# Optimization experiments

Hardware: AMD Instinct MI355X
Metric: run time of the kernel (lower is better)

## Reference

```python
import jax, jax.numpy as jnp
import numpy as np

EPS = 1e-05
KERNEL_SIZE = 9
KERNEL_VOL = float(KERNEL_SIZE ** 3)

_DN = ("NDHWC", "DHWIO", "NDHWC")


def _box_sum(x, k=KERNEL_SIZE):
    """Sliding-window sum over a k^3 box with SAME zero padding.

    The TF module uses a dense all-ones (k,k,k) conv3d; an all-ones kernel is
    separable, so three 1D passes compute the identical result with O(k) work.
    x: (B, D1, D2, D3, 1) float.
    """
    for kshape in ((k, 1, 1), (1, k, 1), (1, 1, k)):
        w = jnp.ones(kshape + (1, 1), dtype=x.dtype)
        x = jax.lax.conv_general_dilated(
            x, w, window_strides=(1, 1, 1), padding="SAME",
            dimension_numbers=_DN)
    return x


def setup_inputs() -> dict:
    key = jax.random.key(0)
    k1, k2 = jax.random.split(key)
    shape = (2, 192, 192, 192)
    y_true = jax.random.uniform(k1, shape, dtype=jnp.float32)
    y_pred = jax.random.uniform(k2, shape, dtype=jnp.float32)
    return {"y_true": y_true, "y_pred": y_pred}


def reference(y_true, y_pred):
    # Expand (B, D1, D2, D3) -> (B, D1, D2, D3, 1) as in the TF call().
    if y_true.ndim == 4:
        y_true = y_true[..., None]
        y_pred = y_pred[..., None]

    t_sum = _box_sum(y_true)
    p_sum = _box_sum(y_pred)
    tp_sum = _box_sum(y_true * y_pred)

    t_avg = t_sum / KERNEL_VOL
    p_avg = p_sum / KERNEL_VOL

    cross = tp_sum - p_avg * t_sum
    num = cross * cross + EPS  # the DEBUG1 variant returns `num` directly
    return num
```

## Files before the change

### kernel.cpp

```cpp
#include <hip/hip_runtime.h>


#define N 192
#define TILE 32
#define ZCHUNK 32
#define NT 6
#define NZC 6

__global__ __launch_bounds__(1024, 4)
void lncc_kernel(const float* __restrict__ t_in,
                 const float* __restrict__ p_in,
                 float* __restrict__ out)
{
    __shared__ __align__(16) float rowT[3 * 32 * 44];
    __shared__ float pcol[3 * 32 * 32];

    const int bid = blockIdx.x;
    const int b   = bid / (NT * NT * NZC);
    int rem       = bid % (NT * NT * NZC);
    const int zc  = rem / (NT * NT);
    rem           = rem % (NT * NT);
    const int ty  = rem / NT;
    const int tx  = rem % NT;

    const int x0 = tx * TILE, y0 = ty * TILE, z0 = zc * ZCHUNK;
    const int tid = threadIdx.x;

    const int  lf   = tid / 320;
    const int  ls   = tid - lf * 320;
    const int  lry  = ls >> 3;
    const int  lxq  = ls & 7;
    const int  lgy  = y0 - 4 + lry;
    const int  lgx0 = x0 - 4 + 4 * lxq;
    const bool lactive = (tid < 960);
    const bool lyok = ((unsigned)lgy < (unsigned)N);

    const int  cf = tid >> 8;
    const int  cyq = (tid >> 5) & 7;
    const int  cx  = tid & 31;
    const bool cactive = (tid < 768);

    const int gx = tid & 31;
    const int gy = tid >> 5;

    const size_t plane = (size_t)N * N;
    const float* tb = t_in + (size_t)b * N * plane;
    const float* pb = p_in + (size_t)b * N * plane;
    float*       ob = out  + (size_t)b * N * plane;

    float ring_t[9], ring_p[9], ring_tp[9];
    float sum_t = 0.f, sum_p = 0.f, sum_tp = 0.f;
    #pragma unroll
    for (int i = 0; i < 9; ++i) { ring_t[i] = 0.f; ring_p[i] = 0.f; ring_tp[i] = 0.f; }

    #pragma unroll 1
    for (int k = 0; k < 5; ++k) {
      #pragma unroll
      for (int r = 0; r < 9; ++r) {
        const int zi = k * 9 + r;
        const int zp = z0 - 4 + zi;
        const bool pvalid = (zi < ZCHUNK + 8) && ((unsigned)zp < (unsigned)N);
        float Pt = 0.f, Pp = 0.f, Ptp = 0.f;
        if (pvalid) {
          if (lactive) {
            const float* rt = tb + (size_t)zp * plane + (size_t)lgy * N;
            const float* rp = pb + (size_t)zp * plane + (size_t)lgy * N;
            float v[12];
            #pragma unroll
            for (int q = 0; q < 3; ++q) {
              const int gxq = lgx0 + 4 * q;
              const bool ok = lyok && ((unsigned)gxq < (unsigned)N);
              float4 a = make_float4(0.f, 0.f, 0.f, 0.f);
              float4 c = make_float4(0.f, 0.f, 0.f, 0.f);
              if (ok) {
                if (lf != 1) a = *(const float4*)(rt + gxq);
                if (lf != 0) c = *(const float4*)(rp + gxq);
              }
              if (lf == 1) a = c;
              if (lf == 2) { a.x *= c.x; a.y *= c.y; a.z *= c.z; a.w *= c.w; }
              v[4*q+0] = a.x; v[4*q+1] = a.y; v[4*q+2] = a.z; v[4*q+3] = a.w;
            }
            float s0 = ((v[0]+v[1]) + (v[2]+v[3])) + ((v[4]+v[5]) + (v[6]+v[7])) + v[8];
            float s1 = s0 - v[0] + v[9];
            float s2 = s1 - v[1] + v[10];
            float s3 = s2 - v[2] + v[11];
            const int wb = (lf * 32 + 4 * lxq) * 44 + lry;
            rowT[wb      ] = s0;
            rowT[wb +  44] = s1;
            rowT[wb +  88] = s2;
            rowT[wb + 132] = s3;
          }
          __syncthreads();
          if (cactive) {
            const float4* rq = (const float4*)&rowT[(cf * 32 + cx) * 44 + 4 * cyq];
            const float4 A = rq[0], B4 = rq[1], C4 = rq[2];
            const float w0=A.x,  w1=A.y,  w2=A.z,  w3=A.w;
            const float w4=B4.x, w5=B4.y, w6=B4.z, w7=B4.w;
            const float w8=C4.x, w9=C4.y, w10=C4.z, w11=C4.w;
            float c0 = ((w0+w1)+(w2+w3)) + ((w4+w5)+(w6+w7)) + w8;
            float c1 = c0 - w0 + w9;
            float c2 = c1 - w1 + w10;
            float c3 = c2 - w2 + w11;
            const int pbase = cf * 1024 + (4 * cyq) * 32 + cx;
            pcol[pbase     ] = c0;
            pcol[pbase + 32] = c1;
            pcol[pbase + 64] = c2;
            pcol[pbase + 96] = c3;
          }
          __syncthreads();
          Pt  = pcol[       gy * 32 + gx];
          Pp  = pcol[1024 + gy * 32 + gx];
          Ptp = pcol[2048 + gy * 32 + gx];
        }
        sum_t  += Pt  - ring_t[r];  ring_t[r]  = Pt;
        sum_p  += Pp  - ring_p[r];  ring_p[r]  = Pp;
        sum_tp += Ptp - ring_tp[r]; ring_tp[r] = Ptp;
        if (zi >= 8 && zi < ZCHUNK + 8) {
          const int zout = zp - 4;
          const float cross = sum_tp - (sum_p * (1.0f / 729.0f)) * sum_t;
          ob[(size_t)zout * plane + (size_t)(y0 + gy) * N + (x0 + gx)]
              = cross * cross + 1e-5f;
        }
      }
    }
}

extern "C" void kernel_launch(void* const* d_in, const int* in_sizes, int n_in,
                              void* d_out, int out_size, void* d_ws, size_t ws_size,
                              hipStream_t stream) {
    const float* y_true = (const float*)d_in[0];
    const float* y_pred = (const float*)d_in[1];
    float* out = (float*)d_out;
    dim3 grid(2 * NT * NT * NZC);
    dim3 block(1024);
    hipLaunchKernelGGL(lncc_kernel, grid, block, 0, stream, y_true, y_pred, out);
}
```

Baseline: 240.6 us.

## Prefetch next z-plane into registers and rebalance z-chunks across a 512-block grid

Loads for plane z+1 are now issued into registers before the shared-memory row/column passes of plane z, so global-load latency overlaps the LDS work and barriers. The grid changes from 432 blocks to 512 blocks with uneven z-chunk sizes (24, 28 or 27 planes), chosen so the block count matches a multiple of the CU count and no wave is left partly idle. The row-transposed LDS stride goes from 44 to 46, with float2 reads, to change the bank-conflict pattern. In exchange it uses more registers for the prefetch buffers and adds more halo recomputation per output plane because the chunks are smaller.

```diff
diff --git a/kernel.cpp b/kernel.cpp
--- a/kernel.cpp
+++ b/kernel.cpp
@@ -2,28 +2,32 @@
 
 
 #define N 192
-#define TILE 32
-#define ZCHUNK 32
-#define NT 6
-#define NZC 6
+#define RSTRIDE 46
 
 __global__ __launch_bounds__(1024, 4)
 void lncc_kernel(const float* __restrict__ t_in,
                  const float* __restrict__ p_in,
                  float* __restrict__ out)
 {
-    __shared__ __align__(16) float rowT[3 * 32 * 44];
+    __shared__ __align__(16) float rowT[3 * 32 * RSTRIDE];
     __shared__ float pcol[3 * 32 * 32];
 
     const int bid = blockIdx.x;
-    const int b   = bid / (NT * NT * NZC);
-    int rem       = bid % (NT * NT * NZC);
-    const int zc  = rem / (NT * NT);
-    rem           = rem % (NT * NT);
-    const int ty  = rem / NT;
-    const int tx  = rem % NT;
-
-    const int x0 = tx * TILE, y0 = ty * TILE, z0 = zc * ZCHUNK;
+    int xy, Z, z0;
+    if (bid < 64) {
+        xy = bid >> 3;
+        Z  = 24;
+        z0 = (bid & 7) * 24;
+    } else {
+        const int q  = bid - 64;
+        xy = 8 + q / 7;
+        const int zi = q % 7;
+        if (zi < 3) { Z = 28; z0 = zi * 28; }
+        else        { Z = 27; z0 = 84 + (zi - 3) * 27; }
+    }
+    const int b  = xy / 36;
+    const int t6 = xy % 36;
+    const int y0 = (t6 / 6) * 32, x0 = (t6 % 6) * 32;
     const int tid = threadIdx.x;
 
     const int  lf   = tid / 320;
@@ -35,7 +39,7 @@
     const bool lactive = (tid < 960);
     const bool lyok = ((unsigned)lgy < (unsigned)N);
 
-    const int  cf = tid >> 8;
+    const int  cf  = tid >> 8;
     const int  cyq = (tid >> 5) & 7;
     const int  cx  = tid & 31;
     const bool cactive = (tid < 768);
@@ -46,80 +50,134 @@
     const size_t plane = (size_t)N * N;
     const float* tb = t_in + (size_t)b * N * plane;
     const float* pb = p_in + (size_t)b * N * plane;
-    float*       ob = out  + (size_t)b * N * plane;
+    float*       ob = out  + (size_t)b * N * plane
+                           + (size_t)(y0 + gy) * N + (x0 + gx);
 
     float ring_t[9], ring_p[9], ring_tp[9];
     float sum_t = 0.f, sum_p = 0.f, sum_tp = 0.f;
     #pragma unroll
     for (int i = 0; i < 9; ++i) { ring_t[i] = 0.f; ring_p[i] = 0.f; ring_tp[i] = 0.f; }
 
+    const float4 z4 = make_float4(0.f, 0.f, 0.f, 0.f);
+    float4 cur0 = z4, cur1 = z4, cur2 = z4;
+
+    {
+        const int zp0 = z0 - 4;
+        if (((unsigned)zp0 < (unsigned)N) && lactive && lyok) {
+            const float* rt = tb + (size_t)zp0 * plane + (size_t)lgy * N;
+            const float* rp = pb + (size_t)zp0 * plane + (size_t)lgy * N;
+            float4 a[3], c[3];
+            #pragma unroll
+            for (int q = 0; q < 3; ++q) {
+                a[q] = z4; c[q] = z4;
+                const int gxq = lgx0 + 4 * q;
+                if ((unsigned)gxq < (unsigned)N) {
+                    a[q] = (lf == 1) ? *(const float4*)(rp + gxq)
+                                     : *(const float4*)(rt + gxq);
+                    if (lf == 2) c[q] = *(const float4*)(rp + gxq);
+                }
+            }
+            if (lf == 2) {
+                #pragma unroll
+                for (int q = 0; q < 3; ++q) {
+                    a[q].x *= c[q].x; a[q].y *= c[q].y;
+                    a[q].z *= c[q].z; a[q].w *= c[q].w;
+                }
+            }
+            cur0 = a[0]; cur1 = a[1]; cur2 = a[2];
+        }
+    }
+
     #pragma unroll 1
-    for (int k = 0; k < 5; ++k) {
+    for (int k = 0; k < 4; ++k) {
       #pragma unroll
       for (int r = 0; r < 9; ++r) {
-        const int zi = k * 9 + r;
-        const int zp = z0 - 4 + zi;
-        const bool pvalid = (zi < ZCHUNK + 8) && ((unsigned)zp < (unsigned)N);
-        float Pt = 0.f, Pp = 0.f, Ptp = 0.f;
-        if (pvalid) {
-          if (lactive) {
-            const float* rt = tb + (size_t)zp * plane + (size_t)lgy * N;
-            const float* rp = pb + (size_t)zp * plane + (size_t)lgy * N;
-            float v[12];
-            #pragma unroll
-            for (int q = 0; q < 3; ++q) {
-              const int gxq = lgx0 + 4 * q;
-              const bool ok = lyok && ((unsigned)gxq < (unsigned)N);
-              float4 a = make_float4(0.f, 0.f, 0.f, 0.f);
-              float4 c = make_float4(0.f, 0.f, 0.f, 0.f);
-              if (ok) {
-                if (lf != 1) a = *(const float4*)(rt + gxq);
-                if (lf != 0) c = *(const float4*)(rp + gxq);
-              }
-              if (lf == 1) a = c;
-              if (lf == 2) { a.x *= c.x; a.y *= c.y; a.z *= c.z; a.w *= c.w; }
-              v[4*q+0] = a.x; v[4*q+1] = a.y; v[4*q+2] = a.z; v[4*q+3] = a.w;
+        const int i  = k * 9 + r;
+        const int zp = z0 - 4 + i;
+        const int zn = zp + 1;
+        const bool vi = (i < Z + 8)     && ((unsigned)zp < (unsigned)N);
+        const bool vn = (i + 1 < Z + 8) && ((unsigned)zn < (unsigned)N);
+
+        float4 fa0 = z4, fa1 = z4, fa2 = z4, fc0 = z4, fc1 = z4, fc2 = z4;
+        if (vn && lactive && lyok) {
+            const float* rt = tb + (size_t)zn * plane + (size_t)lgy * N;
+            const float* rp = pb + (size_t)zn * plane + (size_t)lgy * N;
+            const int g0 = lgx0, g1 = lgx0 + 4, g2 = lgx0 + 8;
+            if ((unsigned)g0 < (unsigned)N) {
+                fa0 = (lf == 1) ? *(const float4*)(rp + g0) : *(const float4*)(rt + g0);
+                if (lf == 2) fc0 = *(const float4*)(rp + g0);
             }
-            float s0 = ((v[0]+v[1]) + (v[2]+v[3])) + ((v[4]+v[5]) + (v[6]+v[7])) + v[8];
-            float s1 = s0 - v[0] + v[9];
-            float s2 = s1 - v[1] + v[10];
-            float s3 = s2 - v[2] + v[11];
-            const int wb = (lf * 32 + 4 * lxq) * 44 + lry;
-            rowT[wb      ] = s0;
-            rowT[wb +  44] = s1;
-            rowT[wb +  88] = s2;
-            rowT[wb + 132] = s3;
-          }
-          __syncthreads();
-          if (cactive) {
-            const float4* rq = (const float4*)&rowT[(cf * 32 + cx) * 44 + 4 * cyq];
-            const float4 A = rq[0], B4 = rq[1], C4 = rq[2];
-            const float w0=A.x,  w1=A.y,  w2=A.z,  w3=A.w;
-            const float w4=B4.x, w5=B4.y, w6=B4.z, w7=B4.w;
-            const float w8=C4.x, w9=C4.y, w10=C4.z, w11=C4.w;
+            if ((unsigned)g1 < (unsigned)N) {
+                fa1 = (lf == 1) ? *(const float4*)(rp + g1) : *(const float4*)(rt + g1);
+                if (lf == 2) fc1 = *(const float4*)(rp + g1);
+            }
+            if ((unsigned)g2 < (unsigned)N) {
+                fa2 = (lf == 1) ? *(const float4*)(rp + g2) : *(const float4*)(rt + g2);
+                if (lf == 2) fc2 = *(const float4*)(rp + g2);
+            }
+        }
+
+        if (vi && lactive) {
+            const float v0 = cur0.x, v1 = cur0.y, v2  = cur0.z, v3  = cur0.w;
+            const float v4 = cur1.x, v5 = cur1.y, v6  = cur1.z, v7  = cur1.w;
+            const float v8 = cur2.x, v9 = cur2.y, v10 = cur2.z, v11 = cur2.w;
+            float s0 = ((v0+v1) + (v2+v3)) + ((v4+v5) + (v6+v7)) + v8;
+            float s1 = s0 - v0 + v9;
+            float s2 = s1 - v1 + v10;
+            float s3 = s2 - v2 + v11;
+            float* wp = &rowT[(lf * 32 + 4 * lxq) * RSTRIDE + lry];
+            wp[0]           = s0;
+            wp[RSTRIDE]     = s1;
+            wp[2 * RSTRIDE] = s2;
+            wp[3 * RSTRIDE] = s3;
+        }
+        __syncthreads();
+
+        if (vi && cactive) {
+            const float* rb = &rowT[(cf * 32 + cx) * RSTRIDE + 4 * cyq];
+            const float2 u0 = *(const float2*)(rb + 0);
+            const float2 u1 = *(const float2*)(rb + 2);
+            const float2 u2 = *(const float2*)(rb + 4);
+            const float2 u3 = *(const float2*)(rb + 6);
+            const float2 u4 = *(const float2*)(rb + 8);
+            const float2 u5 = *(const float2*)(rb + 10);
+            const float w0=u0.x, w1=u0.y, w2=u1.x,  w3=u1.y;
+            const float w4=u2.x, w5=u2.y, w6=u3.x,  w7=u3.y;
+            const float w8=u4.x, w9=u4.y, w10=u5.x, w11=u5.y;
             float c0 = ((w0+w1)+(w2+w3)) + ((w4+w5)+(w6+w7)) + w8;
             float c1 = c0 - w0 + w9;
             float c2 = c1 - w1 + w10;
             float c3 = c2 - w2 + w11;
-            const int pbase = cf * 1024 + (4 * cyq) * 32 + cx;
-            pcol[pbase     ] = c0;
-            pcol[pbase + 32] = c1;
-            pcol[pbase + 64] = c2;
-            pcol[pbase + 96] = c3;
-          }
-          __syncthreads();
-          Pt  = pcol[       gy * 32 + gx];
-          Pp  = pcol[1024 + gy * 32 + gx];
-          Ptp = pcol[2048 + gy * 32 + gx];
+            float* pc = &pcol[cf * 1024 + (4 * cyq) * 32 + cx];
+            pc[0]  = c0;
+            pc[32] = c1;
+            pc[64] = c2;
+            pc[96] = c3;
+        }
+        __syncthreads();
+
+        float Pt = 0.f, Pp = 0.f, Ptp = 0.f;
+        if (vi) {
+            Pt  = pcol[       gy * 32 + gx];
+            Pp  = pcol[1024 + gy * 32 + gx];
+            Ptp = pcol[2048 + gy * 32 + gx];
         }
         sum_t  += Pt  - ring_t[r];  ring_t[r]  = Pt;
         sum_p  += Pp  - ring_p[r];  ring_p[r]  = Pp;
         sum_tp += Ptp - ring_tp[r]; ring_tp[r] = Ptp;
-        if (zi >= 8 && zi < ZCHUNK + 8) {
-          const int zout = zp - 4;
-          const float cross = sum_tp - (sum_p * (1.0f / 729.0f)) * sum_t;
-          ob[(size_t)zout * plane + (size_t)(y0 + gy) * N + (x0 + gx)]
-              = cross * cross + 1e-5f;
+        if (i >= 8 && i < Z + 8) {
+            const float cross = sum_tp - (sum_p * (1.0f / 729.0f)) * sum_t;
+            ob[(size_t)(z0 + i - 8) * plane] = cross * cross + 1e-5f;
+        }
+
+        if (vn && lactive) {
+            float4 A0 = fa0, A1 = fa1, A2 = fa2;
+            if (lf == 2) {
+                A0.x *= fc0.x; A0.y *= fc0.y; A0.z *= fc0.z; A0.w *= fc0.w;
+                A1.x *= fc1.x; A1.y *= fc1.y; A1.z *= fc1.z; A1.w *= fc1.w;
+                A2.x *= fc2.x; A2.y *= fc2.y; A2.z *= fc2.z; A2.w *= fc2.w;
+            }
+            cur0 = A0; cur1 = A1; cur2 = A2;
         }
       }
     }
@@ -131,7 +189,7 @@
     const float* y_true = (const float*)d_in[0];
     const float* y_pred = (const float*)d_in[1];
     float* out = (float*)d_out;
-    dim3 grid(2 * NT * NT * NZC);
+    dim3 grid(512);
     dim3 block(1024);
     hipLaunchKernelGGL(lncc_kernel, grid, block, 0, stream, y_true, y_pred, out);
 }
```

New measurement: 211.9 us. -11.9%, faster.
